# Kernel optimization log

Measured on AMD Instinct MI355X. Metric: run time of the kernel, lower is better.

Reference implementation:

```python
import jax, jax.numpy as jnp
import numpy as np

D_MODEL = 512
B, T = 4, 4096


def setup_inputs() -> dict:
    key = jax.random.key(0)
    k1, k2, k3 = jax.random.split(key, 3)
    x = jax.random.normal(k1, (B, T, D_MODEL), dtype=jnp.float32)
    # torch nn.Linear weight layout: [out_features, in_features]
    w_qkv = jax.random.normal(k2, (3 * D_MODEL, D_MODEL), dtype=jnp.float32) * (1.0 / np.sqrt(D_MODEL))
    w_proj = jax.random.normal(k3, (D_MODEL, D_MODEL), dtype=jnp.float32) * (1.0 / np.sqrt(D_MODEL))
    return {"x": x, "w_qkv": w_qkv, "w_proj": w_proj}


def reference(x, w_qkv, w_proj):
    # Faithful to the torch module: NO head split; attention over full d_model.
    Bx, Tx, C = x.shape
    qkv = jnp.einsum('btc,oc->bto', x, w_qkv)  # [B,T,3C]
    q, k, v = jnp.split(qkv, 3, axis=-1)
    scale = 1.0 / jnp.sqrt(jnp.asarray(C, x.dtype))
    scores = jnp.einsum('btc,bsc->bts', q, k) * scale  # [B,T,T]
    causal = jnp.tril(jnp.ones((Tx, Tx), dtype=bool))
    scores = jnp.where(causal[None, :, :], scores, -jnp.inf)
    weights = jax.nn.softmax(scores, axis=-1)
    out = jnp.einsum('bts,bsc->btc', weights, v)
    return jnp.einsum('btc,oc->bto', out, w_proj)
```

## Files before the change

kernel.cpp:

```cpp
#include <hip/hip_runtime.h>
#include <hip/hip_bf16.h>
#include <stdint.h>

typedef __bf16 bf16_t;
typedef __bf16 bf16x4 __attribute__((ext_vector_type(4)));
typedef __bf16 bf16x8 __attribute__((ext_vector_type(8)));
typedef short s16x4 __attribute__((ext_vector_type(4)));
typedef float f32x4 __attribute__((ext_vector_type(4)));

static_assert(sizeof(bf16x8) == 16, "bf16x8 must be 16B");

#define MFMA_BF16(a, b, c) __builtin_amdgcn_mfma_f32_16x16x32_bf16((a), (b), (c), 0, 0, 0)

__device__ __forceinline__ f32x4 mfma16(bf16x4 a, bf16x4 b, f32x4 c) {
#if __has_builtin(__builtin_amdgcn_mfma_f32_16x16x16bf16_1k)
  union { bf16x4 h; s16x4 s; } ua, ub;
  ua.h = a;
  ub.h = b;
  return __builtin_amdgcn_mfma_f32_16x16x16bf16_1k(ua.s, ub.s, c, 0, 0, 0);
#else
  f32x4 d = c;
  asm volatile("v_mfma_f32_16x16x16_bf16 %0, %1, %2, %0" : "+v"(d) : "v"(a), "v"(b));
  return d;
#endif
}

typedef const __attribute__((address_space(1))) void* gas_ptr;
typedef __attribute__((address_space(3))) void* las_ptr;

__device__ __forceinline__ void gload_lds16(const void* g, void* l) {
  __builtin_amdgcn_global_load_lds((gas_ptr)g, (las_ptr)l, 16, 0, 0);
}

#define ORDER_FENCE() asm volatile("" ::: "memory")

#define NEG_BIG (-1.0e30f)

__global__ __launch_bounds__(256) void cvt3_kernel(
    const float* __restrict__ x, const float* __restrict__ wq,
    const float* __restrict__ wp, bf16_t* __restrict__ xb,
    bf16_t* __restrict__ wqb, bf16_t* __restrict__ wpb) {
  const int i = (blockIdx.x * 256 + threadIdx.x) * 4;
  const float* src;
  bf16_t* dst;
  int off;
  if (i < 8388608) {
    src = x; dst = xb; off = 0;
  } else if (i < 9175040) {
    src = wq; dst = wqb; off = 8388608;
  } else {
    src = wp; dst = wpb; off = 9175040;
  }
  const f32x4 v = *(const f32x4*)(src + (i - off));
  bf16x4 o;
  o[0] = (bf16_t)v[0];
  o[1] = (bf16_t)v[1];
  o[2] = (bf16_t)v[2];
  o[3] = (bf16_t)v[3];
  *(bf16x4*)(dst + (i - off)) = o;
}

template <int MODE>
__global__ __launch_bounds__(256, 2) void gemm_bt_kernel(
    const bf16_t* __restrict__ A, const bf16_t* __restrict__ Bw,
    bf16_t* __restrict__ o_q, bf16_t* __restrict__ o_k, bf16_t* __restrict__ o_vT,
    float* __restrict__ o_f) {
  constexpr int K = 512;
  __shared__ bf16_t As[128 * 32];
  __shared__ bf16_t Bs[128 * 32];

  const int tid = threadIdx.x;
  const int lane = tid & 63;
  const int wid = tid >> 6;
  const int quad = lane >> 4;
  const int l15 = lane & 15;
  const int wm = wid >> 1;
  const int wn = wid & 1;

  const int mt = blockIdx.x & 127;
  const int nt = blockIdx.x >> 7;
  const int row0 = mt * 128;
  const int col0 = nt * 128;

  f32x4 acc[4][4] = {};

  for (int kt = 0; kt < K; kt += 32) {
    __syncthreads();
#pragma unroll
    for (int rnd = 0; rnd < 2; rnd++) {
      const int e = (rnd * 256 + tid) * 8;
      const int r = e >> 5;
      const int c = e & 31;
      gload_lds16(A + (size_t)(row0 + r) * K + kt + c, As + e);
      gload_lds16(Bw + (size_t)(col0 + r) * K + kt + c, Bs + e);
    }
    __syncthreads();

    bf16x8 af[4], bfr[4];
#pragma unroll
    for (int i = 0; i < 4; i++)
      af[i] = *(const bf16x8*)(As + (wm * 64 + i * 16 + l15) * 32 + quad * 8);
#pragma unroll
    for (int i = 0; i < 4; i++)
      bfr[i] = *(const bf16x8*)(Bs + (wn * 64 + i * 16 + l15) * 32 + quad * 8);
#pragma unroll
    for (int mi = 0; mi < 4; mi++)
#pragma unroll
      for (int ni = 0; ni < 4; ni++)
        acc[mi][ni] = MFMA_BF16(af[mi], bfr[ni], acc[mi][ni]);
  }

#pragma unroll
  for (int mi = 0; mi < 4; mi++) {
    const int row = row0 + wm * 64 + mi * 16 + quad * 4;
#pragma unroll
    for (int ni = 0; ni < 4; ni++) {
      const int col = col0 + wn * 64 + ni * 16 + l15;
#pragma unroll
      for (int r = 0; r < 4; r++) {
        const int rr = row + r;
        if constexpr (MODE == 0) {
          const bf16_t bv = (bf16_t)acc[mi][ni][r];
          if (col < 512) {
            o_q[(size_t)rr * 512 + col] = bv;
          } else if (col < 1024) {
            o_k[(size_t)rr * 512 + (col - 512)] = bv;
          } else {
            const int bb = rr >> 12;
            const int t = rr & 4095;
            o_vT[((size_t)bb * 512 + (col - 1024)) * 4096 + t] = bv;
          }
        } else {
          o_f[(size_t)rr * 512 + col] = acc[mi][ni][r];
        }
      }
    }
  }
}

__global__ __launch_bounds__(256, 2) void attn_part_kernel(
    const bf16_t* __restrict__ q, const bf16_t* __restrict__ k,
    const bf16_t* __restrict__ vT, bf16_t* __restrict__ partO,
    float2* __restrict__ stats) {
  __shared__ bf16_t SB[2][16384];

  const int tid = threadIdx.x;
  const int lane = tid & 63;
  const int wid = tid >> 6;
  const int quad = lane >> 4;
  const int l15 = lane & 15;

  const int bid = blockIdx.x;
  const int b = bid & 3;
  const int w = bid >> 2;
  int g = 0;
  while (w >= 4 * (g + 1) * (g + 2)) g++;
  const int rem = w - 4 * g * (g + 1);
  const int i = rem / (g + 1);
  const int c = rem - i * (g + 1);
  const int s = 8 * g + i;

  const int t0w = s * 64 + wid * 16;
  const int kv0 = c * 512;
  const int mmax = min(31, (t0w + 15 - kv0) >> 4);
  const int kvtmax = mmax >> 2;
  const int mmax_blk = min(31, (s * 64 + 63 - kv0) >> 4);
  const int NV = (mmax_blk >> 2) + 1;
  const int NSLICE = 16 + 2 * NV;

  const float scale = 0.044194173824159216f;
  const bf16_t* kbase = k + ((size_t)b * 4096 + kv0) * 512;
  const bf16_t* vbase = vT + ((size_t)b * 512) * 4096 + kv0;

  auto stage_slice = [&](int u, int buf) {
    if (u < 16) {
#pragma unroll
      for (int rnd = 0; rnd < 8; rnd++) {
        const int ch = rnd * 256 + tid;
        const int g4 = ch >> 4;
        const int w16 = ch & 15;
        const int cg = (w16 >> 2) ^ (g4 & 3);
        const int row = g4 * 4 + (w16 & 3);
        gload_lds16(kbase + (size_t)row * 512 + u * 32 + cg * 8,
                    &SB[buf][ch * 8]);
      }
    } else {
      const int v = u - 16;
      const int dh = (v >= NV) ? 1 : 0;
      const int kvt = v - dh * NV;
      const bf16_t* vb = vbase + (size_t)(dh * 256) * 4096;
#pragma unroll
      for (int rnd = 0; rnd < 8; rnd++) {
        const int ch = rnd * 256 + tid;
        const int d = ch >> 3;
        const int cg = (ch & 7) ^ (d & 7);
        gload_lds16(vb + (size_t)d * 4096 + kvt * 64 + cg * 8, &SB[buf][ch * 8]);
      }
    }
  };

  stage_slice(0, 0);
  ORDER_FENCE();
  stage_slice(1, 1);
  ORDER_FENCE();

  bf16x8 qf[16];
  {
    const bf16_t* qp = q + ((size_t)(b * 4096 + t0w + l15)) * 512 + quad * 8;
#pragma unroll
    for (int kk = 0; kk < 16; kk++) qf[kk] = *(const bf16x8*)(qp + kk * 32);
  }

  f32x4 Sacc[32];
#pragma unroll
  for (int m = 0; m < 32; m++) Sacc[m] = f32x4{0.f, 0.f, 0.f, 0.f};

  const int abase =
      ((l15 >> 2) * 16 + (quad ^ ((l15 >> 2) & 3)) * 4 + (l15 & 3)) * 8;

  int cur = 0;
#pragma unroll
  for (int kt = 0; kt < 16; kt++) {
    asm volatile("s_waitcnt vmcnt(8)" ::: "memory");
    __builtin_amdgcn_sched_barrier(0);
    __builtin_amdgcn_s_barrier();
    const bf16_t* sb = &SB[cur][0];
    __builtin_amdgcn_s_setprio(1);
#pragma unroll
    for (int m = 0; m < 32; m++) {
      if (m <= mmax) {
        const bf16x8 kf = *(const bf16x8*)(sb + abase + m * 512);
        Sacc[m] = MFMA_BF16(kf, qf[kt], Sacc[m]);
      }
    }
    __builtin_amdgcn_s_setprio(0);
    asm volatile("s_waitcnt lgkmcnt(0)" ::: "memory");
    __builtin_amdgcn_sched_barrier(0);
    __builtin_amdgcn_s_barrier();
    stage_slice(kt + 2, cur);
    cur ^= 1;
  }

  const int qr = t0w + l15;
  float mx = NEG_BIG;
#pragma unroll
  for (int m = 0; m < 32; m++) {
    if (m <= mmax) {
#pragma unroll
      for (int r = 0; r < 4; r++) {
        const int kv = kv0 + m * 16 + quad * 4 + r;
        const float vvv = (kv <= qr) ? Sacc[m][r] : NEG_BIG;
        Sacc[m][r] = vvv;
        mx = fmaxf(mx, vvv);
      }
    }
  }
  mx = fmaxf(mx, __shfl_xor(mx, 16));
  mx = fmaxf(mx, __shfl_xor(mx, 32));

  float lrow = 0.0f;
  bf16x4 pb[32];
#pragma unroll
  for (int m = 0; m < 32; m++) {
    bf16x4 pv = {};
    if (m <= mmax) {
#pragma unroll
      for (int r = 0; r < 4; r++) {
        const float p = __expf((Sacc[m][r] - mx) * scale);
        pv[r] = (bf16_t)p;
        lrow += p;
      }
    }
    pb[m] = pv;
  }
  lrow += __shfl_xor(lrow, 16);
  lrow += __shfl_xor(lrow, 32);

  if (quad == 0)
    stats[((size_t)w * 4 + b) * 64 + wid * 16 + l15] =
        make_float2(mx * scale, lrow);

  const int l64 = l15 * 64;
  const int qh = quad >> 1;
  const int ql = (quad & 1) * 4;
  const int s7 = l15 & 7;

#pragma unroll
  for (int dh = 0; dh < 2; dh++) {
    f32x4 Oacc[16];
#pragma unroll
    for (int dt = 0; dt < 16; dt++) Oacc[dt] = f32x4{0.f, 0.f, 0.f, 0.f};

#pragma unroll
    for (int kvt = 0; kvt < 8; kvt++) {
      if (kvt < NV) {
        const int u = 16 + dh * NV + kvt;
        if (u < NSLICE - 1)
          asm volatile("s_waitcnt vmcnt(8)" ::: "memory");
        else
          asm volatile("s_waitcnt vmcnt(0)" ::: "memory");
        __builtin_amdgcn_sched_barrier(0);
        __builtin_amdgcn_s_barrier();
        if (kvt <= kvtmax) {
          const bf16_t* sb = &SB[cur][0];
          __builtin_amdgcn_s_setprio(1);
#pragma unroll
          for (int dt = 0; dt < 16; dt++) {
#pragma unroll
            for (int gg = 0; gg < 4; gg++) {
              const bf16x4 vf = *(const bf16x4*)(
                  sb + dt * 1024 + l64 + (((gg * 2 + qh) ^ s7) << 3) + ql);
              Oacc[dt] = mfma16(pb[kvt * 4 + gg], vf, Oacc[dt]);
            }
          }
          __builtin_amdgcn_s_setprio(0);
        }
        if (kvt == NV - 1) {
          bf16_t* pbase =
              partO + (size_t)bid * 32768 + dh * 16384 + wid * 4096;
#pragma unroll
          for (int dt = 0; dt < 16; dt++) {
            bf16x4 ov;
#pragma unroll
            for (int r = 0; r < 4; r++) ov[r] = (bf16_t)Oacc[dt][r];
            *(bf16x4*)(pbase + dt * 256 + l15 * 16 + quad * 4) = ov;
          }
        }
        asm volatile("s_waitcnt lgkmcnt(0)" ::: "memory");
        __builtin_amdgcn_sched_barrier(0);
        __builtin_amdgcn_s_barrier();
        if (u + 2 < NSLICE) stage_slice(u + 2, cur);
        cur ^= 1;
      }
    }
  }
}

__global__ __launch_bounds__(256) void attn_combine_kernel(
    const bf16_t* __restrict__ partO, const float2* __restrict__ stats,
    bf16_t* __restrict__ o) {
  const int b = blockIdx.x & 3;
  const int s = blockIdx.x >> 2;
  const int g = s >> 3;
  const int nc = g + 1;
  const int w0 = 4 * g * (g + 1) + (s & 7) * (g + 1);

  __shared__ float wgt[8][64];
  __shared__ float linv[64];
  __shared__ bf16_t TB[64 * 256];

  const int tid = threadIdx.x;
  if (tid < 64) {
    float mc[8], lc[8];
    float M = NEG_BIG;
    for (int cc = 0; cc < nc; cc++) {
      const float2 ml = stats[((size_t)(w0 + cc) * 4 + b) * 64 + tid];
      mc[cc] = ml.x;
      lc[cc] = ml.y;
      M = fmaxf(M, ml.x);
    }
    float L = 0.0f;
    for (int cc = 0; cc < nc; cc++) {
      const float wv = __expf(mc[cc] - M);
      wgt[cc][tid] = wv;
      L += wv * lc[cc];
    }
    linv[tid] = (L > 0.0f) ? 1.0f / L : 0.0f;
  }
  __syncthreads();

  const int quad = tid & 3;
  const int l15 = (tid >> 2) & 15;
  const int wid = tid >> 6;
  const int q0 = wid * 16 + quad * 4;
  const f32x4 li4 = *(const f32x4*)(&linv[q0]);

  for (int dh = 0; dh < 2; dh++) {
    f32x4 acc4[16] = {};
    for (int cc = 0; cc < nc; cc++) {
      const bf16_t* pp = partO + (size_t)(((w0 + cc) << 2) | b) * 32768 +
                         dh * 16384 + wid * 4096 + l15 * 16 + quad * 4;
      const f32x4 wv4 = *(const f32x4*)(&wgt[cc][q0]);
#pragma unroll
      for (int dt = 0; dt < 16; dt++) {
        const bf16x4 p = *(const bf16x4*)(pp + dt * 256);
#pragma unroll
        for (int e = 0; e < 4; e++) acc4[dt][e] += wv4[e] * (float)p[e];
      }
    }
#pragma unroll
    for (int dt = 0; dt < 16; dt++) {
      const int d2 = (dt * 16 + l15) * 2;
#pragma unroll
      for (int r = 0; r < 4; r++) {
        const int qq = q0 + r;
        *(bf16_t*)((char*)TB + qq * 512 + (d2 ^ ((qq & 7) << 4))) =
            (bf16_t)(acc4[dt][r] * li4[r]);
      }
    }
    __syncthreads();
    const int row = tid >> 2;
    const int quarter = tid & 3;
    bf16_t* orow =
        o + ((size_t)(b * 4096 + s * 64 + row)) * 512 + dh * 256 + quarter * 64;
#pragma unroll
    for (int j = 0; j < 8; j++) {
      const int byte = row * 512 + ((quarter * 128 + j * 16) ^ ((row & 7) << 4));
      *(bf16x8*)(orow + j * 8) = *(const bf16x8*)((const char*)TB + byte);
    }
    __syncthreads();
  }
}

extern "C" void kernel_launch(void* const* d_in, const int* in_sizes, int n_in,
                              void* d_out, int out_size, void* d_ws, size_t ws_size,
                              hipStream_t stream) {
  const float* x_f = (const float*)d_in[0];
  const float* wq_f = (const float*)d_in[1];
  const float* wp_f = (const float*)d_in[2];
  float* out = (float*)d_out;

  bf16_t* xb = (bf16_t*)d_ws;
  bf16_t* wqb = xb + (size_t)16384 * 512;
  bf16_t* wpb = wqb + (size_t)1536 * 512;
  bf16_t* q = wpb + (size_t)512 * 512;
  bf16_t* kk = q + (size_t)16384 * 512;
  bf16_t* vT = kk + (size_t)16384 * 512;
  bf16_t* partO = vT + (size_t)16384 * 512;
  float2* stats = (float2*)(partO + (size_t)1152 * 32768);

  cvt3_kernel<<<9216, 256, 0, stream>>>(x_f, wq_f, wp_f, xb, wqb, wpb);

  gemm_bt_kernel<0><<<128 * 12, 256, 0, stream>>>(xb, wqb, q, kk, vT, nullptr);
  attn_part_kernel<<<1152, 256, 0, stream>>>(q, kk, vT, partO, stats);
  attn_combine_kernel<<<256, 256, 0, stream>>>(partO, stats, xb);
  gemm_bt_kernel<1><<<128 * 4, 256, 0, stream>>>(xb, wpb, nullptr, nullptr, nullptr, out);
}
```

Measured before the change: 435.5 us.

## Switch attention partial kernel to 32x32x16 MFMA with 2x2 wave tiling

Restructures the attention partial kernel to use 32x32x16 bf16 MFMA tiles. The four waves are split 2x2 over queries and KV (for QK^T) and over head-dim halves (for PV). Q is streamed per K-slice instead of held in registers. P is exchanged through a small LDS buffer, and row max and sum are reduced across waves via shared memory. The combine kernel is rewritten to the new partial-output layout and writes all 512 columns in one pass. The aim is higher MFMA throughput per instruction and fewer register-held fragments, at the cost of extra LDS traffic and barriers for the cross-wave softmax and P handoff.

```diff
diff --git a/kernel.cpp b/kernel.cpp
--- a/kernel.cpp
+++ b/kernel.cpp
@@ -5,25 +5,13 @@
 typedef __bf16 bf16_t;
 typedef __bf16 bf16x4 __attribute__((ext_vector_type(4)));
 typedef __bf16 bf16x8 __attribute__((ext_vector_type(8)));
-typedef short s16x4 __attribute__((ext_vector_type(4)));
 typedef float f32x4 __attribute__((ext_vector_type(4)));
+typedef float f32x16 __attribute__((ext_vector_type(16)));
 
 static_assert(sizeof(bf16x8) == 16, "bf16x8 must be 16B");
 
 #define MFMA_BF16(a, b, c) __builtin_amdgcn_mfma_f32_16x16x32_bf16((a), (b), (c), 0, 0, 0)
-
-__device__ __forceinline__ f32x4 mfma16(bf16x4 a, bf16x4 b, f32x4 c) {
-#if __has_builtin(__builtin_amdgcn_mfma_f32_16x16x16bf16_1k)
-  union { bf16x4 h; s16x4 s; } ua, ub;
-  ua.h = a;
-  ub.h = b;
-  return __builtin_amdgcn_mfma_f32_16x16x16bf16_1k(ua.s, ub.s, c, 0, 0, 0);
-#else
-  f32x4 d = c;
-  asm volatile("v_mfma_f32_16x16x16_bf16 %0, %1, %2, %0" : "+v"(d) : "v"(a), "v"(b));
-  return d;
-#endif
-}
+#define MFMA32(a, b, c) __builtin_amdgcn_mfma_f32_32x32x16_bf16((a), (b), (c), 0, 0, 0)
 
 typedef const __attribute__((address_space(1))) void* gas_ptr;
 typedef __attribute__((address_space(3))) void* las_ptr;
@@ -143,12 +131,17 @@
     const bf16_t* __restrict__ vT, bf16_t* __restrict__ partO,
     float2* __restrict__ stats) {
   __shared__ bf16_t SB[2][16384];
+  __shared__ bf16_t PL[2][2048];
+  __shared__ float SMX[2][2][32];
+  __shared__ float SLR[2][2][32];
 
   const int tid = threadIdx.x;
   const int lane = tid & 63;
   const int wid = tid >> 6;
-  const int quad = lane >> 4;
-  const int l15 = lane & 15;
+  const int h = lane >> 5;
+  const int l31 = lane & 31;
+  const int wq = wid & 1;
+  const int wk = wid >> 1;
 
   const int bid = blockIdx.x;
   const int b = bid & 3;
@@ -160,63 +153,46 @@
   const int c = rem - i * (g + 1);
   const int s = 8 * g + i;
 
-  const int t0w = s * 64 + wid * 16;
   const int kv0 = c * 512;
-  const int mmax = min(31, (t0w + 15 - kv0) >> 4);
-  const int kvtmax = mmax >> 2;
-  const int mmax_blk = min(31, (s * 64 + 63 - kv0) >> 4);
-  const int NV = (mmax_blk >> 2) + 1;
-  const int NSLICE = 16 + 2 * NV;
+  const int qmaxw = s * 64 + wq * 32 + 31;
+  const int mtmax = min(7, (qmaxw - kv0 - wk * 256) >> 5);
+  const int NC = min(16, ((s * 64 + 63 - kv0) >> 5) + 1);
 
   const float scale = 0.044194173824159216f;
   const bf16_t* kbase = k + ((size_t)b * 4096 + kv0) * 512;
   const bf16_t* vbase = vT + ((size_t)b * 512) * 4096 + kv0;
-
-  auto stage_slice = [&](int u, int buf) {
-    if (u < 16) {
-#pragma unroll
-      for (int rnd = 0; rnd < 8; rnd++) {
-        const int ch = rnd * 256 + tid;
-        const int g4 = ch >> 4;
-        const int w16 = ch & 15;
-        const int cg = (w16 >> 2) ^ (g4 & 3);
-        const int row = g4 * 4 + (w16 & 3);
-        gload_lds16(kbase + (size_t)row * 512 + u * 32 + cg * 8,
-                    &SB[buf][ch * 8]);
-      }
-    } else {
-      const int v = u - 16;
-      const int dh = (v >= NV) ? 1 : 0;
-      const int kvt = v - dh * NV;
-      const bf16_t* vb = vbase + (size_t)(dh * 256) * 4096;
-#pragma unroll
-      for (int rnd = 0; rnd < 8; rnd++) {
-        const int ch = rnd * 256 + tid;
-        const int d = ch >> 3;
-        const int cg = (ch & 7) ^ (d & 7);
-        gload_lds16(vb + (size_t)d * 4096 + kvt * 64 + cg * 8, &SB[buf][ch * 8]);
-      }
+  const bf16_t* qp =
+      q + ((size_t)(b * 4096 + s * 64 + wq * 32 + l31)) * 512 + h * 8;
+
+  auto stageK = [&](int kt, int buf) {
+#pragma unroll
+    for (int rnd = 0; rnd < 8; rnd++) {
+      const int ch = rnd * 256 + tid;
+      const int mg = ch >> 7, kk2 = (ch >> 6) & 1, hk = (ch >> 5) & 1, l = ch & 31;
+      gload_lds16(kbase + (size_t)(mg * 32 + l) * 512 + kt * 32 + kk2 * 16 + hk * 8,
+                  &SB[buf][ch * 8]);
     }
   };
-
-  stage_slice(0, 0);
+  auto stageV = [&](int cc, int buf) {
+#pragma unroll
+    for (int rnd = 0; rnd < 8; rnd++) {
+      const int ch = rnd * 256 + tid;
+      const int dg = ch >> 7, c2 = (ch >> 6) & 1, hv = (ch >> 5) & 1, l = ch & 31;
+      gload_lds16(vbase + (size_t)(dg * 32 + l) * 4096 + cc * 32 + c2 * 16 + hv * 8,
+                  &SB[buf][ch * 8]);
+    }
+  };
+
+  bf16x8 qbuf[2][2];
+  qbuf[0][0] = *(const bf16x8*)(qp + 0);
+  qbuf[0][1] = *(const bf16x8*)(qp + 16);
   ORDER_FENCE();
-  stage_slice(1, 1);
+  stageK(0, 0);
   ORDER_FENCE();
-
-  bf16x8 qf[16];
-  {
-    const bf16_t* qp = q + ((size_t)(b * 4096 + t0w + l15)) * 512 + quad * 8;
-#pragma unroll
-    for (int kk = 0; kk < 16; kk++) qf[kk] = *(const bf16x8*)(qp + kk * 32);
-  }
-
-  f32x4 Sacc[32];
-#pragma unroll
-  for (int m = 0; m < 32; m++) Sacc[m] = f32x4{0.f, 0.f, 0.f, 0.f};
-
-  const int abase =
-      ((l15 >> 2) * 16 + (quad ^ ((l15 >> 2) & 3)) * 4 + (l15 & 3)) * 8;
+  stageK(1, 1);
+  ORDER_FENCE();
+
+  f32x16 Sacc[8] = {};
 
   int cur = 0;
 #pragma unroll
@@ -227,111 +203,137 @@
     const bf16_t* sb = &SB[cur][0];
     __builtin_amdgcn_s_setprio(1);
 #pragma unroll
-    for (int m = 0; m < 32; m++) {
-      if (m <= mmax) {
-        const bf16x8 kf = *(const bf16x8*)(sb + abase + m * 512);
-        Sacc[m] = MFMA_BF16(kf, qf[kt], Sacc[m]);
+    for (int kk2 = 0; kk2 < 2; kk2++) {
+#pragma unroll
+      for (int mt = 0; mt < 8; mt++) {
+        if (mt <= mtmax) {
+          const bf16x8 kf = *(const bf16x8*)(
+              sb + (wk * 8 + mt) * 1024 + kk2 * 512 + h * 256 + l31 * 8);
+          Sacc[mt] = MFMA32(kf, qbuf[kt & 1][kk2], Sacc[mt]);
+        }
       }
     }
     __builtin_amdgcn_s_setprio(0);
     asm volatile("s_waitcnt lgkmcnt(0)" ::: "memory");
     __builtin_amdgcn_sched_barrier(0);
     __builtin_amdgcn_s_barrier();
-    stage_slice(kt + 2, cur);
+    if (kt < 15) {
+      qbuf[(kt + 1) & 1][0] = *(const bf16x8*)(qp + (kt + 1) * 32);
+      qbuf[(kt + 1) & 1][1] = *(const bf16x8*)(qp + (kt + 1) * 32 + 16);
+      ORDER_FENCE();
+    }
+    if (kt < 14)
+      stageK(kt + 2, cur);
+    else
+      stageV(kt - 14, cur);
     cur ^= 1;
   }
 
-  const int qr = t0w + l15;
+  const int qr = s * 64 + wq * 32 + l31;
   float mx = NEG_BIG;
 #pragma unroll
-  for (int m = 0; m < 32; m++) {
-    if (m <= mmax) {
-#pragma unroll
-      for (int r = 0; r < 4; r++) {
-        const int kv = kv0 + m * 16 + quad * 4 + r;
-        const float vvv = (kv <= qr) ? Sacc[m][r] : NEG_BIG;
-        Sacc[m][r] = vvv;
-        mx = fmaxf(mx, vvv);
+  for (int mt = 0; mt < 8; mt++) {
+    if (mt <= mtmax) {
+#pragma unroll
+      for (int rr = 0; rr < 4; rr++)
+#pragma unroll
+        for (int j = 0; j < 4; j++) {
+          const int kvg = kv0 + wk * 256 + mt * 32 + 8 * rr + 4 * h + j;
+          if (kvg <= qr) mx = fmaxf(mx, Sacc[mt][rr * 4 + j]);
+        }
+    }
+  }
+  mx = fmaxf(mx, __shfl_xor(mx, 32));
+  if (lane < 32) SMX[wq][wk][l31] = mx;
+  asm volatile("s_waitcnt lgkmcnt(0)" ::: "memory");
+  __builtin_amdgcn_sched_barrier(0);
+  __builtin_amdgcn_s_barrier();
+  const float M = fmaxf(SMX[wq][0][l31], SMX[wq][1][l31]);
+
+  float lrow = 0.0f;
+  bf16x4 pb[8][4] = {};
+#pragma unroll
+  for (int mt = 0; mt < 8; mt++) {
+    if (mt <= mtmax) {
+#pragma unroll
+      for (int rr = 0; rr < 4; rr++) {
+        bf16x4 pv = {};
+#pragma unroll
+        for (int j = 0; j < 4; j++) {
+          const int kvg = kv0 + wk * 256 + mt * 32 + 8 * rr + 4 * h + j;
+          float p = 0.0f;
+          if (kvg <= qr) p = __expf((Sacc[mt][rr * 4 + j] - M) * scale);
+          pv[j] = (bf16_t)p;
+          lrow += p;
+        }
+        pb[mt][rr] = pv;
       }
     }
   }
-  mx = fmaxf(mx, __shfl_xor(mx, 16));
-  mx = fmaxf(mx, __shfl_xor(mx, 32));
-
-  float lrow = 0.0f;
-  bf16x4 pb[32];
-#pragma unroll
-  for (int m = 0; m < 32; m++) {
-    bf16x4 pv = {};
-    if (m <= mmax) {
-#pragma unroll
-      for (int r = 0; r < 4; r++) {
-        const float p = __expf((Sacc[m][r] - mx) * scale);
-        pv[r] = (bf16_t)p;
-        lrow += p;
+  lrow += __shfl_xor(lrow, 32);
+  if (lane < 32) SLR[wq][wk][l31] = lrow;
+  asm volatile("s_waitcnt lgkmcnt(0)" ::: "memory");
+  __builtin_amdgcn_sched_barrier(0);
+  __builtin_amdgcn_s_barrier();
+  const float L = SLR[wq][0][l31] + SLR[wq][1][l31];
+  if (wk == 0 && lane < 32)
+    stats[((size_t)w * 4 + b) * 64 + wq * 32 + l31] = make_float2(M * scale, L);
+
+  auto pwrite = [&](int mt, int buf) {
+#pragma unroll
+    for (int rr = 0; rr < 4; rr++) {
+      *(bf16x4*)((char*)&PL[buf][0] + wq * 2048 + (rr >> 1) * 1024 +
+                 (rr & 1) * 512 + l31 * 16 + 8 * h) = pb[mt][rr];
+    }
+  };
+  if (wk == 0) pwrite(0, 0);
+  asm volatile("s_waitcnt lgkmcnt(0)" ::: "memory");
+  __builtin_amdgcn_sched_barrier(0);
+  __builtin_amdgcn_s_barrier();
+
+  const int dh = wk;
+  f32x16 Oacc[8] = {};
+#pragma unroll
+  for (int cc = 0; cc < 16; cc++) {
+    if (cc < NC) {
+      if (cc == NC - 1)
+        asm volatile("s_waitcnt vmcnt(0)" ::: "memory");
+      else
+        asm volatile("s_waitcnt vmcnt(8)" ::: "memory");
+      __builtin_amdgcn_sched_barrier(0);
+      __builtin_amdgcn_s_barrier();
+      const bf16_t* sb = &SB[cur][0];
+      __builtin_amdgcn_s_setprio(1);
+#pragma unroll
+      for (int c2 = 0; c2 < 2; c2++) {
+        const bf16x8 pA = *(const bf16x8*)(
+            (const char*)&PL[cc & 1][0] + wq * 2048 + c2 * 1024 + h * 512 + l31 * 16);
+#pragma unroll
+        for (int dt = 0; dt < 8; dt++) {
+          const bf16x8 vB = *(const bf16x8*)(
+              sb + (dh * 8 + dt) * 1024 + c2 * 512 + h * 256 + l31 * 8);
+          Oacc[dt] = MFMA32(pA, vB, Oacc[dt]);
+        }
       }
-    }
-    pb[m] = pv;
-  }
-  lrow += __shfl_xor(lrow, 16);
-  lrow += __shfl_xor(lrow, 32);
-
-  if (quad == 0)
-    stats[((size_t)w * 4 + b) * 64 + wid * 16 + l15] =
-        make_float2(mx * scale, lrow);
-
-  const int l64 = l15 * 64;
-  const int qh = quad >> 1;
-  const int ql = (quad & 1) * 4;
-  const int s7 = l15 & 7;
-
-#pragma unroll
-  for (int dh = 0; dh < 2; dh++) {
-    f32x4 Oacc[16];
-#pragma unroll
-    for (int dt = 0; dt < 16; dt++) Oacc[dt] = f32x4{0.f, 0.f, 0.f, 0.f};
-
-#pragma unroll
-    for (int kvt = 0; kvt < 8; kvt++) {
-      if (kvt < NV) {
-        const int u = 16 + dh * NV + kvt;
-        if (u < NSLICE - 1)
-          asm volatile("s_waitcnt vmcnt(8)" ::: "memory");
-        else
-          asm volatile("s_waitcnt vmcnt(0)" ::: "memory");
-        __builtin_amdgcn_sched_barrier(0);
-        __builtin_amdgcn_s_barrier();
-        if (kvt <= kvtmax) {
-          const bf16_t* sb = &SB[cur][0];
-          __builtin_amdgcn_s_setprio(1);
-#pragma unroll
-          for (int dt = 0; dt < 16; dt++) {
-#pragma unroll
-            for (int gg = 0; gg < 4; gg++) {
-              const bf16x4 vf = *(const bf16x4*)(
-                  sb + dt * 1024 + l64 + (((gg * 2 + qh) ^ s7) << 3) + ql);
-              Oacc[dt] = mfma16(pb[kvt * 4 + gg], vf, Oacc[dt]);
-            }
-          }
-          __builtin_amdgcn_s_setprio(0);
-        }
-        if (kvt == NV - 1) {
-          bf16_t* pbase =
-              partO + (size_t)bid * 32768 + dh * 16384 + wid * 4096;
-#pragma unroll
-          for (int dt = 0; dt < 16; dt++) {
-            bf16x4 ov;
-#pragma unroll
-            for (int r = 0; r < 4; r++) ov[r] = (bf16_t)Oacc[dt][r];
-            *(bf16x4*)(pbase + dt * 256 + l15 * 16 + quad * 4) = ov;
-          }
-        }
-        asm volatile("s_waitcnt lgkmcnt(0)" ::: "memory");
-        __builtin_amdgcn_sched_barrier(0);
-        __builtin_amdgcn_s_barrier();
-        if (u + 2 < NSLICE) stage_slice(u + 2, cur);
-        cur ^= 1;
-      }
+      __builtin_amdgcn_s_setprio(0);
+      if (cc + 1 < NC && wk == ((cc + 1) >> 3)) pwrite((cc + 1) & 7, (cc + 1) & 1);
+      asm volatile("s_waitcnt lgkmcnt(0)" ::: "memory");
+      __builtin_amdgcn_sched_barrier(0);
+      __builtin_amdgcn_s_barrier();
+      if (cc + 2 < NC) stageV(cc + 2, cur);
+      cur ^= 1;
+    }
+  }
+
+  bf16_t* pbase = partO + (size_t)bid * 32768 + (size_t)(dh * 2 + wq) * 8192;
+#pragma unroll
+  for (int dt = 0; dt < 8; dt++) {
+#pragma unroll
+    for (int rr = 0; rr < 4; rr++) {
+      bf16x4 ov;
+#pragma unroll
+      for (int j = 0; j < 4; j++) ov[j] = (bf16_t)Oacc[dt][rr * 4 + j];
+      *(bf16x4*)(pbase + dt * 1024 + rr * 256 + h * 128 + l31 * 4) = ov;
     }
   }
 }
@@ -347,7 +349,7 @@
 
   __shared__ float wgt[8][64];
   __shared__ float linv[64];
-  __shared__ bf16_t TB[64 * 256];
+  __shared__ bf16_t TB[64 * 512];
 
   const int tid = threadIdx.x;
   if (tid < 64) {
@@ -369,46 +371,42 @@
   }
   __syncthreads();
 
-  const int quad = tid & 3;
-  const int l15 = (tid >> 2) & 15;
-  const int wid = tid >> 6;
-  const int q0 = wid * 16 + quad * 4;
-  const f32x4 li4 = *(const f32x4*)(&linv[q0]);
-
-  for (int dh = 0; dh < 2; dh++) {
-    f32x4 acc4[16] = {};
+  const int rr = tid >> 6;
+  const int hh = (tid >> 5) & 1;
+  const int l31 = tid & 31;
+
+  for (int seg = 0; seg < 32; seg++) {
+    const int dh = seg >> 4;
+    const int wqq = (seg >> 3) & 1;
+    const int dt = seg & 7;
+    const int q0 = wqq * 32 + 8 * rr + 4 * hh;
+    const int d = dh * 256 + dt * 32 + l31;
+    f32x4 acc = {};
     for (int cc = 0; cc < nc; cc++) {
-      const bf16_t* pp = partO + (size_t)(((w0 + cc) << 2) | b) * 32768 +
-                         dh * 16384 + wid * 4096 + l15 * 16 + quad * 4;
-      const f32x4 wv4 = *(const f32x4*)(&wgt[cc][q0]);
-#pragma unroll
-      for (int dt = 0; dt < 16; dt++) {
-        const bf16x4 p = *(const bf16x4*)(pp + dt * 256);
-#pragma unroll
-        for (int e = 0; e < 4; e++) acc4[dt][e] += wv4[e] * (float)p[e];
-      }
-    }
-#pragma unroll
-    for (int dt = 0; dt < 16; dt++) {
-      const int d2 = (dt * 16 + l15) * 2;
-#pragma unroll
-      for (int r = 0; r < 4; r++) {
-        const int qq = q0 + r;
-        *(bf16_t*)((char*)TB + qq * 512 + (d2 ^ ((qq & 7) << 4))) =
-            (bf16_t)(acc4[dt][r] * li4[r]);
-      }
-    }
-    __syncthreads();
-    const int row = tid >> 2;
-    const int quarter = tid & 3;
-    bf16_t* orow =
-        o + ((size_t)(b * 4096 + s * 64 + row)) * 512 + dh * 256 + quarter * 64;
-#pragma unroll
-    for (int j = 0; j < 8; j++) {
-      const int byte = row * 512 + ((quarter * 128 + j * 16) ^ ((row & 7) << 4));
-      *(bf16x8*)(orow + j * 8) = *(const bf16x8*)((const char*)TB + byte);
-    }
-    __syncthreads();
+      const int bidc = ((w0 + cc) << 2) | b;
+      const bf16x4 p = *(const bf16x4*)(partO + (size_t)bidc * 32768 +
+                                        (size_t)(seg * 256 + tid) * 4);
+      const f32x4 wv = *(const f32x4*)(&wgt[cc][q0]);
+#pragma unroll
+      for (int e = 0; e < 4; e++) acc[e] += wv[e] * (float)p[e];
+    }
+    const f32x4 li = *(const f32x4*)(&linv[q0]);
+#pragma unroll
+    for (int j = 0; j < 4; j++) {
+      const int qq = q0 + j;
+      *(bf16_t*)((char*)TB + qq * 1024 + ((d * 2) ^ ((qq & 7) << 4))) =
+          (bf16_t)(acc[j] * li[j]);
+    }
+  }
+  __syncthreads();
+
+  const int row = tid >> 2;
+  const int dq = (tid & 3) * 128;
+  bf16_t* orow = o + ((size_t)(b * 4096 + s * 64 + row)) * 512 + dq;
+#pragma unroll
+  for (int jj = 0; jj < 16; jj++) {
+    const int byte = row * 1024 + (((dq + jj * 8) * 2) ^ ((row & 7) << 4));
+    *(bf16x8*)(orow + jj * 8) = *(const bf16x8*)((const char*)TB + byte);
   }
 }
 
```

Result: slower. 464.1 us (+6.6%).
